# Performance work log

Measured on AMD Instinct MI355X. Metric: run time of the kernel, lower is better.

## Reference

```python
import jax, jax.numpy as jnp
import numpy as np
from jax import lax

H = W = 128            # feature map spatial size (2h x 2w)
WIN = 16               # attention window size
DIM = 512
HEADS = 8
DIM_HEAD = 64
INNER = HEADS * DIM_HEAD
SCALE = DIM_HEAD ** -0.5
KEEP = 44
IOU_T = 0.2

_s = np.arange(0, H - WIN + 1, WIN // 2)
_sx, _sy = np.meshgrid(_s, _s)
WINDOWS = np.stack([_sx.ravel(), _sy.ravel(), _sx.ravel() + WIN - 1, _sy.ravel() + WIN - 1], 1).astype(np.float32)
M = WINDOWS.shape[0]   # 225
SX = jnp.asarray(WINDOWS[:, 0].astype(np.int32))
SY = jnp.asarray(WINDOWS[:, 1].astype(np.int32))

# ---- static pairwise IoU (torchvision convention: area=(x2-x1)*(y2-y1)) ----
_x1, _y1, _x2, _y2 = WINDOWS[:, 0], WINDOWS[:, 1], WINDOWS[:, 2], WINDOWS[:, 3]
_area = (_x2 - _x1) * (_y2 - _y1)
_iw = np.clip(np.minimum(_x2[:, None], _x2[None]) - np.maximum(_x1[:, None], _x1[None]), 0, None)
_ih = np.clip(np.minimum(_y2[:, None], _y2[None]) - np.maximum(_y1[:, None], _y1[None]), 0, None)
_inter = _iw * _ih
IOU = jnp.asarray((_inter / (_area[:, None] + _area[None] - _inter)).astype(np.float32))

# ---- roi_align (aligned=False, 1 sample/bin) == separable bilinear resample ----
_bin = (WIN - 1.0) / WIN
_r = (np.arange(WIN) + 0.5) * _bin
_q = np.floor(_r).astype(int)
_f = _r - _q
_A = np.zeros((WIN, WIN), np.float32)
_A[np.arange(WIN), _q] = 1.0 - _f
_A[np.arange(WIN), np.minimum(_q + 1, WIN - 1)] += _f
BILIN = jnp.asarray(_A)


def _nms_select(score):
    """Greedy NMS over the static window set; return first KEEP kept indices."""
    order = jnp.argsort(-score)
    iou_s = IOU[order][:, order]
    def body(i, supp):
        return supp | ((~supp[i]) & (iou_s[i] > IOU_T) & (jnp.arange(M) > i))
    supp = lax.fori_loop(0, M, body, jnp.zeros((M,), dtype=bool))
    pos = jnp.where(~supp, jnp.arange(M), M)
    pos = jnp.minimum(jnp.sort(pos)[:KEEP], M - 1)
    return order[pos]


def setup_inputs() -> dict:
    key = jax.random.key(0)
    k1, k2, k3, k4 = jax.random.split(key, 4)
    x = jax.random.normal(k1, (8, H * W, DIM), dtype=jnp.float32)
    prob = jax.random.uniform(k2, (8, 4, H // 2, W // 2), dtype=jnp.float32)
    W_fix = jnp.ones((1, 1, WIN // 2, WIN // 2), jnp.float32)   # FixCNN ones kernel
    W_qkv = jax.random.normal(k3, (3 * INNER, DIM), jnp.float32) * 0.02
    W_out = jax.random.normal(k4, (DIM, INNER), jnp.float32) * 0.02
    b_out = jnp.zeros((DIM,), jnp.float32)
    return {"x": x, "prob": prob, "W_fix": W_fix, "W_qkv": W_qkv, "W_out": W_out, "b_out": b_out}


def reference(x, prob, W_fix, W_qkv, W_out, b_out):
    b = x.shape[0]
    # entropy over class channels
    entropy = -jnp.sum(prob * jnp.log2(prob + 1e-10), axis=1)           # (b, 64, 64)
    # FixCNN: ones 8x8 kernel, stride 4, then /64
    score = lax.conv(entropy[:, None], W_fix, (WIN // 4, WIN // 4), 'VALID')
    score = (score / float((WIN // 2) ** 2)).reshape(b, -1)             # (b, M)
    x2d = x.transpose(0, 2, 1).reshape(b, DIM, H, W)                    # b d h w
    rng = jnp.arange(WIN)

    def per_batch(feat, sc):
        idx = _nms_select(sc)                                           # (KEEP,)
        sy, sx = SY[idx], SX[idx]
        # gather integer 16x16 patches (box corners are integers)
        patches = jax.vmap(lambda y, xc: lax.dynamic_slice(feat, (0, y, xc), (DIM, WIN, WIN)))(sy, sx)
        # roi_align bilinear resample (separable)
        pat = jnp.einsum('pi,mdij,qj->mdpq', BILIN, patches, BILIN)     # (KEEP, d, 16, 16)
        xi = pat.transpose(0, 2, 3, 1).reshape(KEEP, WIN * WIN, DIM)    # m n d
        qkv = xi @ W_qkv.T
        q, k, v = jnp.split(qkv, 3, axis=-1)
        to_h = lambda t: t.reshape(KEEP, WIN * WIN, HEADS, DIM_HEAD).transpose(0, 2, 1, 3)
        q, k, v = to_h(q), to_h(k), to_h(v)
        attn = jax.nn.softmax(jnp.einsum('mhnd,mhkd->mhnk', q, k) * SCALE, axis=-1)
        out = jnp.einsum('mhnk,mhkd->mhnd', attn, v)
        out = out.transpose(0, 2, 1, 3).reshape(KEEP, WIN * WIN, INNER)
        out = out @ W_out.T + b_out                                     # (KEEP, n, DIM)
        out2d = out.reshape(KEEP, WIN, WIN, DIM).transpose(0, 3, 1, 2)  # m d h w
        yy = sy[:, None, None] + rng[None, :, None]                     # (KEEP,16,1)
        xx = sx[:, None, None] + rng[None, None, :]                     # (KEEP,1,16)
        acc = jnp.zeros((DIM, H, W), x.dtype).at[:, yy, xx].add(out2d.transpose(1, 0, 2, 3))
        cnt = jnp.zeros((H, W), x.dtype).at[yy, xx].add(1.0)
        return acc, cnt

    acc, cnt = jax.vmap(per_batch)(x2d, score)
    outx = (acc / (cnt[:, None] + 1e-10)).reshape(b, DIM, H * W).transpose(0, 2, 1)
    return x + outx
```

## Files before the change

### kernel.cpp

```cpp
#include <hip/hip_runtime.h>
#include <type_traits>
#include <utility>

typedef unsigned short u16;
typedef __attribute__((ext_vector_type(8))) short short8;
typedef __attribute__((ext_vector_type(8))) __bf16 bf16v8;
typedef __attribute__((ext_vector_type(4))) float f32x4;
typedef __attribute__((ext_vector_type(16))) float f32x16;

template <typename T, typename = void> struct mfma_ok : std::false_type {};
template <typename T>
struct mfma_ok<T, std::void_t<decltype(__builtin_amdgcn_mfma_f32_16x16x32_bf16(
    std::declval<T>(), std::declval<T>(), std::declval<f32x4>(), 0, 0, 0))>>
    : std::true_type {};
using frag8 = std::conditional_t<mfma_ok<bf16v8>::value, bf16v8, short8>;

#define MFMA16(a, b, c) __builtin_amdgcn_mfma_f32_16x16x32_bf16((a), (b), (c), 0, 0, 0)
#define MFMA32(a, b, c) __builtin_amdgcn_mfma_f32_32x32x16_bf16((a), (b), (c), 0, 0, 0)

__device__ __forceinline__ float bf2f(u16 u) {
  unsigned v = ((unsigned)u) << 16;
  return __builtin_bit_cast(float, v);
}
__device__ __forceinline__ u16 f2bf(float f) {
  unsigned u = __builtin_bit_cast(unsigned, f);
  u = (u + 0x7fffu + ((u >> 16) & 1u)) >> 16;
  return (u16)u;
}
__device__ __forceinline__ unsigned cvtpk_bf16(float lo, float hi) {
  unsigned r;
  asm("v_cvt_pk_bf16_f32 %0, %1, %2" : "=v"(r) : "v"(lo), "v"(hi));
  return r;
}
__device__ __forceinline__ void gl16(const u16* g, u16* l) {
  __builtin_amdgcn_global_load_lds((__attribute__((address_space(1))) void*)(g),
                                   (__attribute__((address_space(3))) void*)(l), 16, 0, 0);
}
__device__ __forceinline__ void vmw8() { asm volatile("s_waitcnt vmcnt(8)" ::: "memory"); }
__device__ __forceinline__ void vmw0() { asm volatile("s_waitcnt vmcnt(0)" ::: "memory"); }
__device__ __forceinline__ void lgw0() { asm volatile("s_waitcnt lgkmcnt(0)" ::: "memory"); }


__global__ void k_score(const float* __restrict__ prob, const float* __restrict__ wfix,
                        float* __restrict__ scores) {
  const int b = blockIdx.x, tid = threadIdx.x;
  __shared__ float ent[64 * 64];
  __shared__ float wf[64];
  if (tid < 64) wf[tid] = wfix[tid];
  const float* pb = prob + (size_t)b * 4 * 4096;
  for (int p = tid; p < 4096; p += 256) {
    float e = 0.f;
#pragma unroll
    for (int ch = 0; ch < 4; ++ch) {
      float v = pb[ch * 4096 + p];
      e -= v * log2f(v + 1e-10f);
    }
    ent[p] = e;
  }
  __syncthreads();
  if (tid < 225) {
    int wy = tid / 15, wx = tid % 15;
    float s = 0.f;
    for (int a = 0; a < 8; ++a)
      for (int c = 0; c < 8; ++c)
        s += ent[(wy * 4 + a) * 64 + wx * 4 + c] * wf[a * 8 + c];
    scores[b * 225 + tid] = s * (1.0f / 64.0f);
  }
}

__device__ __forceinline__ float iou_pair(int wa, int wb) {
  float x1a = (float)((wa % 15) * 8), y1a = (float)((wa / 15) * 8);
  float x1b = (float)((wb % 15) * 8), y1b = (float)((wb / 15) * 8);
  float iw = fminf(x1a, x1b) + 15.f - fmaxf(x1a, x1b);
  float ih = fminf(y1a, y1b) + 15.f - fmaxf(y1a, y1b);
  iw = fmaxf(iw, 0.f);
  ih = fmaxf(ih, 0.f);
  float inter = iw * ih;
  return inter / (450.f - inter);
}

__global__ void k_nms(const float* __restrict__ scores, int* __restrict__ sel,
                      int* __restrict__ kept, float* __restrict__ mult) {
  const int b = blockIdx.x, t = threadIdx.x;
  __shared__ float s[225];
  __shared__ int order[225];
  __shared__ unsigned char supp[225];
  __shared__ int idx44[44];
  __shared__ int ks[225];
  __shared__ float ml[225];
  if (t < 225) s[t] = scores[b * 225 + t];
  __syncthreads();
  if (t < 225) {
    float st = s[t];
    int r = 0;
    for (int j = 0; j < 225; ++j) {
      float sj = s[j];
      r += (sj > st) || (sj == st && j < t);
    }
    order[r] = t;
    supp[t] = 0;
    ks[t] = -1;
    ml[t] = 0.f;
  }
  __syncthreads();
  for (int i = 0; i < 224; ++i) {
    if (t > i && t < 225 && !supp[i]) {
      if (iou_pair(order[i], order[t]) > 0.2f) supp[t] = 1;
    }
    __syncthreads();
  }
  if (t == 0) {
    int k = 0;
    for (int i = 0; i < 225 && k < 44; ++i)
      if (!supp[i]) idx44[k++] = order[i];
    while (k < 44) idx44[k++] = order[224];
    for (int k2 = 0; k2 < 44; ++k2) {
      int w = idx44[k2];
      if (ks[w] < 0) ks[w] = k2;
      ml[w] += 1.f;
    }
  }
  __syncthreads();
  if (t < 225) {
    kept[b * 225 + t] = ks[t];
    mult[b * 225 + t] = ml[t];
  }
  if (t < 44) sel[b * 44 + t] = idx44[t];
}

__global__ void k_castw(const float* __restrict__ Wq, const float* __restrict__ Wo,
                        u16* __restrict__ wqb, u16* __restrict__ wob) {
  int idx = blockIdx.x * 256 + threadIdx.x;
  if (idx < 786432) wqb[idx] = f2bf(Wq[idx]);
  int i2 = idx - 786432;
  if (i2 >= 0 && i2 < 262144) wob[i2] = f2bf(Wo[i2]);
}

__global__ __launch_bounds__(256) void k_gather(const float* __restrict__ x,
                                                const int* __restrict__ sel,
                                                u16* __restrict__ xi) {
  const size_t idx = (size_t)blockIdx.x * 256 + threadIdx.x;
  const int dc = (int)(idx & 63);
  const int pq = (int)((idx >> 6) & 255);
  const int g = (int)(idx >> 14);
  const int b = g / 44;
  const int w = sel[g];
  const int sy = (w / 15) * 8, sx = (w % 15) * 8;
  const int p = pq >> 4, q = pq & 15;
  float rp = ((float)p + 0.5f) * 0.9375f;
  int i0 = (int)rp;
  float fp = rp - (float)i0;
  float rq = ((float)q + 0.5f) * 0.9375f;
  int j0 = (int)rq;
  float fq = rq - (float)j0;
  const float w00 = (1.f - fp) * (1.f - fq), w01 = (1.f - fp) * fq;
  const float w10 = fp * (1.f - fq), w11 = fp * fq;
  const float* xb = x + ((size_t)b * 16384 + (size_t)(sy + i0) * 128 + sx + j0) * 512 + dc * 8;
  const float4* t00 = (const float4*)xb;
  const float4* t01 = (const float4*)(xb + 512);
  const float4* t10 = (const float4*)(xb + 512 * 128);
  const float4* t11 = (const float4*)(xb + 512 * 129);
  float acc[8];
#pragma unroll
  for (int h = 0; h < 2; ++h) {
    float4 a = t00[h], bb = t01[h], c = t10[h], d = t11[h];
    acc[h * 4 + 0] = w00 * a.x + w01 * bb.x + w10 * c.x + w11 * d.x;
    acc[h * 4 + 1] = w00 * a.y + w01 * bb.y + w10 * c.y + w11 * d.y;
    acc[h * 4 + 2] = w00 * a.z + w01 * bb.z + w10 * c.z + w11 * d.z;
    acc[h * 4 + 3] = w00 * a.w + w01 * bb.w + w10 * c.w + w11 * d.w;
  }
  short8 o;
#pragma unroll
  for (int e = 0; e < 8; ++e) o[e] = (short)f2bf(acc[e]);
  *(short8*)&xi[((size_t)g * 256 + pq) * 512 + dc * 8] = o;
}

template <int BIAS, int OPERM, int APERM>
__global__ __launch_bounds__(256, 2) void k_gemm128(const u16* __restrict__ A,
                                                    const u16* __restrict__ B, u16* __restrict__ C,
                                                    const float* __restrict__ bias, int M, int N,
                                                    int K, int nbn) {
  __shared__ u16 sA[2][128 * 64];
  __shared__ u16 sB[2][128 * 64];
  const int tid = threadIdx.x, lane = tid & 63, wv = tid >> 6;
  const int f = blockIdx.x;
  const int q8 = gridDim.x >> 3;
  const int wg = (f & 7) * q8 + (f >> 3);
  const int bm = wg / nbn, bn = wg % nbn;
  const int wm = (wv >> 1) * 64, wn = (wv & 1) * 64;
  const int l15 = lane & 15, k8 = (lane >> 4) * 8;
  const int xorv = (l15 & 7) * 8;
  const int srow = tid >> 3;
  const int sc8 = ((tid ^ (tid >> 3)) & 7) * 8;
  const int arow0 = bm * 128 + srow, brow0 = bn * 128 + srow;

  f32x4 acc[4][4] = {};

#define STAGE(kt, buf)                                                                          \
  {                                                                                             \
    _Pragma("unroll") for (int c = 0; c < 4; ++c) {                                             \
      const int ar = arow0 + c * 32;                                                            \
      size_t aoffs = APERM ? ((size_t)(ar >> 8) * 131072 + (size_t)(kt) * 16384 +               \
                              (size_t)(ar & 255) * 64 + sc8)                                    \
                           : ((size_t)ar * K + (kt) * 64 + sc8);                                \
      gl16(A + aoffs, &sA[buf][c * 2048 + wv * 512]);                                           \
      gl16(B + (size_t)(brow0 + c * 32) * K + (kt) * 64 + sc8, &sB[buf][c * 2048 + wv * 512]); \
    }                                                                                           \
  }

  STAGE(0, 0);
  STAGE(1, 1);

  for (int t = 0; t < 8; ++t) {
    const int buf = t & 1;
    if (t == 7)
      vmw0();
    else
      vmw8();
    __builtin_amdgcn_sched_barrier(0);
    __builtin_amdgcn_s_barrier();
    frag8 af[4][2], bf[4][2];
#pragma unroll
    for (int i = 0; i < 4; ++i)
#pragma unroll
      for (int kk = 0; kk < 2; ++kk) {
        af[i][kk] = *(const frag8*)&sA[buf][(wm + i * 16 + l15) * 64 + ((kk * 32 + k8) ^ xorv)];
        bf[i][kk] = *(const frag8*)&sB[buf][(wn + i * 16 + l15) * 64 + ((kk * 32 + k8) ^ xorv)];
      }
    __builtin_amdgcn_s_setprio(1);
#pragma unroll
    for (int i = 0; i < 4; ++i)
#pragma unroll
      for (int j = 0; j < 4; ++j)
#pragma unroll
        for (int kk = 0; kk < 2; ++kk)
          acc[i][j] = MFMA16(af[i][kk], bf[j][kk], acc[i][j]);
    __builtin_amdgcn_s_setprio(0);
    lgw0();
    __builtin_amdgcn_sched_barrier(0);
    __builtin_amdgcn_s_barrier();
    if (t < 6) STAGE(t + 2, buf);
  }
#undef STAGE

  const int cc = lane & 15, rr = (lane >> 4) * 4;
#pragma unroll
  for (int i = 0; i < 4; ++i)
#pragma unroll
    for (int j = 0; j < 4; ++j) {
      int col = bn * 128 + wn + j * 16 + cc;
      float badd = BIAS ? bias[col] : 0.f;
#pragma unroll
      for (int e = 0; e < 4; ++e) {
        int row = bm * 128 + wm + i * 16 + rr + e;
        if (OPERM) {
          size_t caddr = (size_t)(row >> 8) * 393216 + (size_t)(col >> 9) * 131072 +
                         (size_t)((col >> 6) & 7) * 16384 + (size_t)(row & 255) * 64 + (col & 63);
          C[caddr] = f2bf(acc[i][j][e] + badd);
        } else {
          C[(size_t)row * N + col] = f2bf(acc[i][j][e] + badd);
        }
      }
    }
}

__global__ __launch_bounds__(256, 3) void k_attn(const u16* __restrict__ qkv,
                                                 u16* __restrict__ aout) {
  const int g = blockIdx.x;
  const int win = g % 352, h = g / 352;
  const int tid = threadIdx.x, lane = tid & 63, wv = tid >> 6;
  const int l31 = lane & 31, l5 = lane >> 5;
  __shared__ u16 smem[17664];
  u16* KbB = smem;
  u16* VtB = smem + 8704;
  const u16* qbase = qkv + (size_t)win * 393216 + (size_t)h * 16384;
  const u16* kbase = qbase + 131072;
  const u16* vbase = qbase + 262144;
  const int prow = tid >> 2, pc16 = (tid & 3) * 16;

  frag8 qf[2][4];
#pragma unroll
  for (int qt = 0; qt < 2; ++qt)
#pragma unroll
    for (int c = 0; c < 4; ++c)
      qf[qt][c] = *(const frag8*)(qbase + (size_t)(wv * 64 + qt * 32 + l31) * 64 + c * 16 +
                                  l5 * 8);
  {
    const u16* kp = kbase + (size_t)prow * 64 + pc16;
    short8 ka = *(const short8*)kp;
    short8 kb2 = *(const short8*)(kp + 8);
    const u16* vp = vbase + (size_t)prow * 64 + pc16;
    short8 va = *(const short8*)vp;
    short8 vb2 = *(const short8*)(vp + 8);
    *(short8*)&KbB[prow * 68 + pc16] = ka;
    *(short8*)&KbB[prow * 68 + pc16 + 8] = kb2;
#pragma unroll
    for (int e = 0; e < 8; ++e) {
      VtB[(pc16 + e) * 70 + prow] = (u16)va[e];
      VtB[(pc16 + 8 + e) * 70 + prow] = (u16)vb2[e];
    }
  }
  __syncthreads();

  f32x16 of[2][2] = {};
  float m_run[2] = {-3e38f, -3e38f};
  float l_run[2] = {0.f, 0.f};

  int cur = 0;
  for (int kb = 0; kb < 4; ++kb) {
    short8 pk0 = {}, pk1 = {}, pv0 = {}, pv1 = {};
    if (kb < 3) {
      const u16* kp = kbase + (size_t)((kb + 1) * 64 + prow) * 64 + pc16;
      pk0 = *(const short8*)kp;
      pk1 = *(const short8*)(kp + 8);
      const u16* vp = vbase + (size_t)((kb + 1) * 64 + prow) * 64 + pc16;
      pv0 = *(const short8*)vp;
      pv1 = *(const short8*)(vp + 8);
    }
#pragma unroll
    for (int qt = 0; qt < 2; ++qt) {
      f32x16 s0 = {}, s1 = {};
#pragma unroll
      for (int c = 0; c < 4; ++c) {
        frag8 kf0 = *(const frag8*)&KbB[cur * 4352 + l31 * 68 + c * 16 + l5 * 8];
        frag8 kf1 = *(const frag8*)&KbB[cur * 4352 + (32 + l31) * 68 + c * 16 + l5 * 8];
        s0 = MFMA32(kf0, qf[qt][c], s0);
        s1 = MFMA32(kf1, qf[qt][c], s1);
      }
      float tm[16];
#pragma unroll
      for (int r = 0; r < 16; ++r) tm[r] = fmaxf(s0[r], s1[r]);
#pragma unroll
      for (int r = 0; r < 8; ++r) tm[r] = fmaxf(tm[r], tm[r + 8]);
#pragma unroll
      for (int r = 0; r < 4; ++r) tm[r] = fmaxf(tm[r], tm[r + 4]);
      float pm = fmaxf(fmaxf(tm[0], tm[1]), fmaxf(tm[2], tm[3]));
      pm = fmaxf(pm, __shfl_xor(pm, 32));
      if (!__all(pm <= m_run[qt] + 64.f)) {
        float mn = fmaxf(m_run[qt], pm);
        float corr = __expf((m_run[qt] - mn) * 0.125f);
        l_run[qt] *= corr;
#pragma unroll
        for (int dt = 0; dt < 2; ++dt)
#pragma unroll
          for (int r = 0; r < 16; ++r) of[qt][dt][r] *= corr;
        m_run[qt] = mn;
      }
      const float mqt = m_run[qt];
      float ls = 0.f;
#pragma unroll
      for (int kt = 0; kt < 2; ++kt) {
        const f32x16 sv = kt ? s1 : s0;
        float p[16];
#pragma unroll
        for (int r = 0; r < 16; ++r) p[r] = __expf((sv[r] - mqt) * 0.125f);
        float e0 = (p[0] + p[1]) + (p[2] + p[3]);
        float e1 = (p[4] + p[5]) + (p[6] + p[7]);
        float e2 = (p[8] + p[9]) + (p[10] + p[11]);
        float e3 = (p[12] + p[13]) + (p[14] + p[15]);
        ls += (e0 + e1) + (e2 + e3);
#pragma unroll
        for (int cc = 0; cc < 2; ++cc) {
          const int bx = cc * 8;
          unsigned a0 = cvtpk_bf16(p[bx + 0], p[bx + 1]);
          unsigned a1 = cvtpk_bf16(p[bx + 2], p[bx + 3]);
          unsigned b0 = cvtpk_bf16(p[bx + 4], p[bx + 5]);
          unsigned b1 = cvtpk_bf16(p[bx + 6], p[bx + 7]);
          asm("v_permlane32_swap_b32 %0, %1" : "+v"(a0), "+v"(b0));
          asm("v_permlane32_swap_b32 %0, %1" : "+v"(a1), "+v"(b1));
          uint4 fu;
          fu.x = a0;
          fu.y = a1;
          fu.z = b0;
          fu.w = b1;
          frag8 pb = __builtin_bit_cast(frag8, fu);
#pragma unroll
          for (int dt = 0; dt < 2; ++dt) {
            frag8 va = *(const frag8*)&VtB[cur * 4480 + (dt * 32 + l31) * 70 + kt * 32 + cc * 16 +
                                           l5 * 8];
            of[qt][dt] = MFMA32(va, pb, of[qt][dt]);
          }
        }
      }
      l_run[qt] += ls;
    }
    if (kb < 3) {
      *(short8*)&KbB[(cur ^ 1) * 4352 + prow * 68 + pc16] = pk0;
      *(short8*)&KbB[(cur ^ 1) * 4352 + prow * 68 + pc16 + 8] = pk1;
      u16* vd = &VtB[(cur ^ 1) * 4480 + prow];
#pragma unroll
      for (int e = 0; e < 8; ++e) {
        vd[(pc16 + e) * 70] = (u16)pv0[e];
        vd[(pc16 + 8 + e) * 70] = (u16)pv1[e];
      }
    }
    __syncthreads();
    cur ^= 1;
  }

  float inv[2];
#pragma unroll
  for (int qt = 0; qt < 2; ++qt) {
    float lt = l_run[qt] + __shfl_xor(l_run[qt], 32);
    inv[qt] = 1.0f / lt;
  }
  u16* sc = smem + wv * 4352;
  __syncthreads();
#pragma unroll
  for (int qt = 0; qt < 2; ++qt)
#pragma unroll
    for (int dt = 0; dt < 2; ++dt)
#pragma unroll
      for (int j = 0; j < 4; ++j) {
        unsigned w0 = cvtpk_bf16(of[qt][dt][4 * j + 0] * inv[qt], of[qt][dt][4 * j + 1] * inv[qt]);
        unsigned w1 = cvtpk_bf16(of[qt][dt][4 * j + 2] * inv[qt], of[qt][dt][4 * j + 3] * inv[qt]);
        *(uint2*)&sc[(qt * 32 + l31) * 68 + dt * 32 + 8 * j + 4 * l5] = make_uint2(w0, w1);
      }
  asm volatile("" ::: "memory");
  u16* obase = aout + (size_t)win * 131072 + (size_t)h * 16384 + (size_t)wv * 64 * 64;
#pragma unroll
  for (int rep = 0; rep < 8; ++rep) {
    int row = rep * 8 + (lane >> 3);
    uint2 lo = *(const uint2*)&sc[row * 68 + (lane & 7) * 8];
    uint2 hi = *(const uint2*)&sc[row * 68 + (lane & 7) * 8 + 4];
    *(int4*)&obase[(size_t)row * 64 + (lane & 7) * 8] =
        make_int4((int)lo.x, (int)lo.y, (int)hi.x, (int)hi.y);
  }
}

__global__ void k_final(const float* __restrict__ x, const u16* __restrict__ proj,
                        const int* __restrict__ kept, const float* __restrict__ mult,
                        float* __restrict__ out) {
  const size_t idx = (size_t)blockIdx.x * 256 + threadIdx.x;
  const int dci = (int)(idx & 31);
  const int pix = (int)((idx >> 5) & 16383);
  const int b = (int)(idx >> 19);
  const int y = pix >> 7, xc = pix & 127;
  float acc[16];
#pragma unroll
  for (int e = 0; e < 16; ++e) acc[e] = 0.f;
  float c = 0.f;
  const int wyh = y >> 3, wxh = xc >> 3;
#pragma unroll
  for (int a = 0; a < 2; ++a) {
    int wy = wyh - 1 + a;
    if (wy < 0 || wy > 14) continue;
#pragma unroll
    for (int bb = 0; bb < 2; ++bb) {
      int wx = wxh - 1 + bb;
      if (wx < 0 || wx > 14) continue;
      int w = wy * 15 + wx;
      int slot = kept[b * 225 + w];
      if (slot < 0) continue;
      float ml = mult[b * 225 + w];
      c += ml;
      const u16* pr = proj +
                      ((size_t)((b * 44 + slot) * 256 + (y - wy * 8) * 16 + (xc - wx * 8))) * 512 +
                      (size_t)dci * 16;
      short8 v0 = *(const short8*)pr;
      short8 v1 = *(const short8*)(pr + 8);
#pragma unroll
      for (int e = 0; e < 8; ++e) acc[e] += ml * bf2f((u16)v0[e]);
#pragma unroll
      for (int e = 0; e < 8; ++e) acc[8 + e] += ml * bf2f((u16)v1[e]);
    }
  }
  const float inv = 1.f / (c + 1e-10f);
  const size_t off = ((size_t)(b * 16384 + pix)) * 512 + (size_t)dci * 16;
  const float4* xp = (const float4*)(x + off);
  float4* op = (float4*)(out + off);
#pragma unroll
  for (int q4 = 0; q4 < 4; ++q4) {
    float4 xv = xp[q4];
    float4 ov;
    ov.x = xv.x + acc[q4 * 4 + 0] * inv;
    ov.y = xv.y + acc[q4 * 4 + 1] * inv;
    ov.z = xv.z + acc[q4 * 4 + 2] * inv;
    ov.w = xv.w + acc[q4 * 4 + 3] * inv;
    op[q4] = ov;
  }
}

extern "C" void kernel_launch(void* const* d_in, const int* in_sizes, int n_in, void* d_out,
                              int out_size, void* d_ws, size_t ws_size, hipStream_t stream) {
  const float* x = (const float*)d_in[0];
  const float* prob = (const float*)d_in[1];
  const float* wfix = (const float*)d_in[2];
  const float* Wq = (const float*)d_in[3];
  const float* Wo = (const float*)d_in[4];
  const float* bo = (const float*)d_in[5];
  float* out = (float*)d_out;
  char* ws = (char*)d_ws;

  float* scores = (float*)(ws + 0);
  int* sel = (int*)(ws + 8192);
  int* kept = (int*)(ws + 16384);
  float* mult = (float*)(ws + 24576);
  u16* wqb = (u16*)(ws + 32768);
  u16* wob = (u16*)(ws + 32768 + 1572864);
  u16* xi = (u16*)(ws + 4194304);
  u16* qkv = (u16*)(ws + 4194304 + 92274688);
  u16* aout = xi;
  u16* proj = qkv;

  k_score<<<8, 256, 0, stream>>>(prob, wfix, scores);
  k_nms<<<8, 256, 0, stream>>>(scores, sel, kept, mult);
  k_castw<<<4096, 256, 0, stream>>>(Wq, Wo, wqb, wob);
  k_gather<<<22528, 256, 0, stream>>>(x, sel, xi);
  k_gemm128<0, 1, 0><<<8448, 256, 0, stream>>>(xi, wqb, qkv, nullptr, 90112, 1536, 512, 12);
  k_attn<<<2816, 256, 0, stream>>>(qkv, aout);
  k_gemm128<1, 0, 1><<<2816, 256, 0, stream>>>(aout, wob, proj, bo, 90112, 512, 512, 4);
  k_final<<<16384, 256, 0, stream>>>(x, proj, kept, mult, out);
}
```

Measured before the change: 747.8 us.

## Split attention query rows across two blocks per window-head to double grid

Each attention block now handles 128 query rows (32 per wave) instead of 256, doubling the grid to 5632 blocks and raising launch bounds to 4 blocks per CU. This cuts per-thread registers (one query tile instead of two) and aims to improve occupancy and latency hiding. In exchange, K and V for each window-head are loaded and transposed into shared memory twice, adding global and LDS traffic.

```diff
diff --git a/kernel.cpp b/kernel.cpp
--- a/kernel.cpp
+++ b/kernel.cpp
@@ -264,10 +264,12 @@
     }
 }
 
-__global__ __launch_bounds__(256, 3) void k_attn(const u16* __restrict__ qkv,
+__global__ __launch_bounds__(256, 4) void k_attn(const u16* __restrict__ qkv,
                                                  u16* __restrict__ aout) {
   const int g = blockIdx.x;
-  const int win = g % 352, h = g / 352;
+  const int win = g % 352;
+  const int hq = g / 352;
+  const int h = hq & 7, qh = hq >> 3;
   const int tid = threadIdx.x, lane = tid & 63, wv = tid >> 6;
   const int l31 = lane & 31, l5 = lane >> 5;
   __shared__ u16 smem[17664];
@@ -277,14 +279,12 @@
   const u16* kbase = qbase + 131072;
   const u16* vbase = qbase + 262144;
   const int prow = tid >> 2, pc16 = (tid & 3) * 16;
-
-  frag8 qf[2][4];
-#pragma unroll
-  for (int qt = 0; qt < 2; ++qt)
-#pragma unroll
-    for (int c = 0; c < 4; ++c)
-      qf[qt][c] = *(const frag8*)(qbase + (size_t)(wv * 64 + qt * 32 + l31) * 64 + c * 16 +
-                                  l5 * 8);
+  const int qrow0 = qh * 128 + wv * 32;
+
+  frag8 qf[4];
+#pragma unroll
+  for (int c = 0; c < 4; ++c)
+    qf[c] = *(const frag8*)(qbase + (size_t)(qrow0 + l31) * 64 + c * 16 + l5 * 8);
   {
     const u16* kp = kbase + (size_t)prow * 64 + pc16;
     short8 ka = *(const short8*)kp;
@@ -302,9 +302,9 @@
   }
   __syncthreads();
 
-  f32x16 of[2][2] = {};
-  float m_run[2] = {-3e38f, -3e38f};
-  float l_run[2] = {0.f, 0.f};
+  f32x16 of[2] = {};
+  float m_run = -3e38f;
+  float l_run = 0.f;
 
   int cur = 0;
   for (int kb = 0; kb < 4; ++kb) {
@@ -317,73 +317,70 @@
       pv0 = *(const short8*)vp;
       pv1 = *(const short8*)(vp + 8);
     }
-#pragma unroll
-    for (int qt = 0; qt < 2; ++qt) {
-      f32x16 s0 = {}, s1 = {};
-#pragma unroll
-      for (int c = 0; c < 4; ++c) {
-        frag8 kf0 = *(const frag8*)&KbB[cur * 4352 + l31 * 68 + c * 16 + l5 * 8];
-        frag8 kf1 = *(const frag8*)&KbB[cur * 4352 + (32 + l31) * 68 + c * 16 + l5 * 8];
-        s0 = MFMA32(kf0, qf[qt][c], s0);
-        s1 = MFMA32(kf1, qf[qt][c], s1);
-      }
-      float tm[16];
-#pragma unroll
-      for (int r = 0; r < 16; ++r) tm[r] = fmaxf(s0[r], s1[r]);
-#pragma unroll
-      for (int r = 0; r < 8; ++r) tm[r] = fmaxf(tm[r], tm[r + 8]);
-#pragma unroll
-      for (int r = 0; r < 4; ++r) tm[r] = fmaxf(tm[r], tm[r + 4]);
-      float pm = fmaxf(fmaxf(tm[0], tm[1]), fmaxf(tm[2], tm[3]));
-      pm = fmaxf(pm, __shfl_xor(pm, 32));
-      if (!__all(pm <= m_run[qt] + 64.f)) {
-        float mn = fmaxf(m_run[qt], pm);
-        float corr = __expf((m_run[qt] - mn) * 0.125f);
-        l_run[qt] *= corr;
-#pragma unroll
-        for (int dt = 0; dt < 2; ++dt)
-#pragma unroll
-          for (int r = 0; r < 16; ++r) of[qt][dt][r] *= corr;
-        m_run[qt] = mn;
-      }
-      const float mqt = m_run[qt];
-      float ls = 0.f;
-#pragma unroll
-      for (int kt = 0; kt < 2; ++kt) {
-        const f32x16 sv = kt ? s1 : s0;
-        float p[16];
-#pragma unroll
-        for (int r = 0; r < 16; ++r) p[r] = __expf((sv[r] - mqt) * 0.125f);
-        float e0 = (p[0] + p[1]) + (p[2] + p[3]);
-        float e1 = (p[4] + p[5]) + (p[6] + p[7]);
-        float e2 = (p[8] + p[9]) + (p[10] + p[11]);
-        float e3 = (p[12] + p[13]) + (p[14] + p[15]);
-        ls += (e0 + e1) + (e2 + e3);
-#pragma unroll
-        for (int cc = 0; cc < 2; ++cc) {
-          const int bx = cc * 8;
-          unsigned a0 = cvtpk_bf16(p[bx + 0], p[bx + 1]);
-          unsigned a1 = cvtpk_bf16(p[bx + 2], p[bx + 3]);
-          unsigned b0 = cvtpk_bf16(p[bx + 4], p[bx + 5]);
-          unsigned b1 = cvtpk_bf16(p[bx + 6], p[bx + 7]);
-          asm("v_permlane32_swap_b32 %0, %1" : "+v"(a0), "+v"(b0));
-          asm("v_permlane32_swap_b32 %0, %1" : "+v"(a1), "+v"(b1));
-          uint4 fu;
-          fu.x = a0;
-          fu.y = a1;
-          fu.z = b0;
-          fu.w = b1;
-          frag8 pb = __builtin_bit_cast(frag8, fu);
-#pragma unroll
-          for (int dt = 0; dt < 2; ++dt) {
-            frag8 va = *(const frag8*)&VtB[cur * 4480 + (dt * 32 + l31) * 70 + kt * 32 + cc * 16 +
-                                           l5 * 8];
-            of[qt][dt] = MFMA32(va, pb, of[qt][dt]);
-          }
+    f32x16 s0 = {}, s1 = {};
+#pragma unroll
+    for (int c = 0; c < 4; ++c) {
+      frag8 kf0 = *(const frag8*)&KbB[cur * 4352 + l31 * 68 + c * 16 + l5 * 8];
+      frag8 kf1 = *(const frag8*)&KbB[cur * 4352 + (32 + l31) * 68 + c * 16 + l5 * 8];
+      s0 = MFMA32(kf0, qf[c], s0);
+      s1 = MFMA32(kf1, qf[c], s1);
+    }
+    float tm[16];
+#pragma unroll
+    for (int r = 0; r < 16; ++r) tm[r] = fmaxf(s0[r], s1[r]);
+#pragma unroll
+    for (int r = 0; r < 8; ++r) tm[r] = fmaxf(tm[r], tm[r + 8]);
+#pragma unroll
+    for (int r = 0; r < 4; ++r) tm[r] = fmaxf(tm[r], tm[r + 4]);
+    float pm = fmaxf(fmaxf(tm[0], tm[1]), fmaxf(tm[2], tm[3]));
+    pm = fmaxf(pm, __shfl_xor(pm, 32));
+    if (!__all(pm <= m_run + 64.f)) {
+      float mn = fmaxf(m_run, pm);
+      float corr = __expf((m_run - mn) * 0.125f);
+      l_run *= corr;
+#pragma unroll
+      for (int dt = 0; dt < 2; ++dt)
+#pragma unroll
+        for (int r = 0; r < 16; ++r) of[dt][r] *= corr;
+      m_run = mn;
+    }
+    const float mqt = m_run;
+    float ls = 0.f;
+#pragma unroll
+    for (int kt = 0; kt < 2; ++kt) {
+      const f32x16 sv = kt ? s1 : s0;
+      float p[16];
+#pragma unroll
+      for (int r = 0; r < 16; ++r) p[r] = __expf((sv[r] - mqt) * 0.125f);
+      float e0 = (p[0] + p[1]) + (p[2] + p[3]);
+      float e1 = (p[4] + p[5]) + (p[6] + p[7]);
+      float e2 = (p[8] + p[9]) + (p[10] + p[11]);
+      float e3 = (p[12] + p[13]) + (p[14] + p[15]);
+      ls += (e0 + e1) + (e2 + e3);
+#pragma unroll
+      for (int cc = 0; cc < 2; ++cc) {
+        const int bx = cc * 8;
+        unsigned a0 = cvtpk_bf16(p[bx + 0], p[bx + 1]);
+        unsigned a1 = cvtpk_bf16(p[bx + 2], p[bx + 3]);
+        unsigned b0 = cvtpk_bf16(p[bx + 4], p[bx + 5]);
+        unsigned b1 = cvtpk_bf16(p[bx + 6], p[bx + 7]);
+        asm("v_permlane32_swap_b32 %0, %1" : "+v"(a0), "+v"(b0));
+        asm("v_permlane32_swap_b32 %0, %1" : "+v"(a1), "+v"(b1));
+        uint4 fu;
+        fu.x = a0;
+        fu.y = a1;
+        fu.z = b0;
+        fu.w = b1;
+        frag8 pb = __builtin_bit_cast(frag8, fu);
+#pragma unroll
+        for (int dt = 0; dt < 2; ++dt) {
+          frag8 va = *(const frag8*)&VtB[cur * 4480 + (dt * 32 + l31) * 70 + kt * 32 + cc * 16 +
+                                         l5 * 8];
+          of[dt] = MFMA32(va, pb, of[dt]);
         }
       }
-      l_run[qt] += ls;
-    }
+    }
+    l_run += ls;
     if (kb < 3) {
       *(short8*)&KbB[(cur ^ 1) * 4352 + prow * 68 + pc16] = pk0;
       *(short8*)&KbB[(cur ^ 1) * 4352 + prow * 68 + pc16 + 8] = pk1;
@@ -398,28 +395,22 @@
     cur ^= 1;
   }
 
-  float inv[2];
-#pragma unroll
-  for (int qt = 0; qt < 2; ++qt) {
-    float lt = l_run[qt] + __shfl_xor(l_run[qt], 32);
-    inv[qt] = 1.0f / lt;
-  }
-  u16* sc = smem + wv * 4352;
+  float lt = l_run + __shfl_xor(l_run, 32);
+  float inv = 1.0f / lt;
+  u16* sc = smem + wv * 2176;
   __syncthreads();
 #pragma unroll
-  for (int qt = 0; qt < 2; ++qt)
-#pragma unroll
-    for (int dt = 0; dt < 2; ++dt)
-#pragma unroll
-      for (int j = 0; j < 4; ++j) {
-        unsigned w0 = cvtpk_bf16(of[qt][dt][4 * j + 0] * inv[qt], of[qt][dt][4 * j + 1] * inv[qt]);
-        unsigned w1 = cvtpk_bf16(of[qt][dt][4 * j + 2] * inv[qt], of[qt][dt][4 * j + 3] * inv[qt]);
-        *(uint2*)&sc[(qt * 32 + l31) * 68 + dt * 32 + 8 * j + 4 * l5] = make_uint2(w0, w1);
-      }
+  for (int dt = 0; dt < 2; ++dt)
+#pragma unroll
+    for (int j = 0; j < 4; ++j) {
+      unsigned w0 = cvtpk_bf16(of[dt][4 * j + 0] * inv, of[dt][4 * j + 1] * inv);
+      unsigned w1 = cvtpk_bf16(of[dt][4 * j + 2] * inv, of[dt][4 * j + 3] * inv);
+      *(uint2*)&sc[l31 * 68 + dt * 32 + 8 * j + 4 * l5] = make_uint2(w0, w1);
+    }
   asm volatile("" ::: "memory");
-  u16* obase = aout + (size_t)win * 131072 + (size_t)h * 16384 + (size_t)wv * 64 * 64;
-#pragma unroll
-  for (int rep = 0; rep < 8; ++rep) {
+  u16* obase = aout + (size_t)win * 131072 + (size_t)h * 16384 + (size_t)qrow0 * 64;
+#pragma unroll
+  for (int rep = 0; rep < 4; ++rep) {
     int row = rep * 8 + (lane >> 3);
     uint2 lo = *(const uint2*)&sc[row * 68 + (lane & 7) * 8];
     uint2 hi = *(const uint2*)&sc[row * 68 + (lane & 7) * 8 + 4];
@@ -508,7 +499,7 @@
   k_castw<<<4096, 256, 0, stream>>>(Wq, Wo, wqb, wob);
   k_gather<<<22528, 256, 0, stream>>>(x, sel, xi);
   k_gemm128<0, 1, 0><<<8448, 256, 0, stream>>>(xi, wqb, qkv, nullptr, 90112, 1536, 512, 12);
-  k_attn<<<2816, 256, 0, stream>>>(qkv, aout);
+  k_attn<<<5632, 256, 0, stream>>>(qkv, aout);
   k_gemm128<1, 0, 1><<<2816, 256, 0, stream>>>(aout, wob, proj, bo, 90112, 512, 512, 4);
   k_final<<<16384, 256, 0, stream>>>(x, proj, kept, mult, out);
 }
```

After: 742.4 us. Within noise of the previous version (-0.7%).
